# Kernel tuning notes

Hardware: AMD Instinct MI355X
Metric: run time of the kernel (lower is better)

The kernel has to match this reference:

```python
import jax, jax.numpy as jnp
import numpy as np
import math

B, L, X, E, Y = 2, 1024, 4, 128, 4  # batch, win_size/seq, search heads, head dim, retrieval heads


def setup_inputs() -> dict:
    key = jax.random.key(0)
    ks = jax.random.split(key, 12)
    f = jnp.float32
    x = jax.random.normal(ks[0], (B, L, X, E), f)
    query = jax.random.normal(ks[1], (B, L, X, E), f)
    k = jax.random.normal(ks[2], (B, L, X, E), f)
    value = jax.random.normal(ks[3], (B, L, Y, E), f)
    sigma = jax.random.normal(ks[4], (B, L, X), f)
    q_plus = jax.random.normal(ks[5], (B, L, X, E), f)
    # custom triangular mask over (search, retrieval) dims, broadcastable to scores [B,L,M,X,Y]
    attn_mask = jnp.triu(jnp.ones((X, Y), dtype=bool), k=1)
    # Linear(E,E) params (key_plus projection and V projection)
    s = 1.0 / math.sqrt(E)
    Wk = jax.random.normal(ks[6], (E, E), f) * s
    bk = jax.random.normal(ks[7], (E,), f) * s
    Wv = jax.random.normal(ks[8], (E, E), f) * s
    bv = jax.random.normal(ks[9], (E,), f) * s
    return {"x": x, "query": query, "key": k, "value": value, "sigma": sigma,
            "attn_mask": attn_mask, "retrieval": Y, "search": X, "q_plus": q_plus,
            "Wk": Wk, "bk": bk, "Wv": Wv, "bv": bv}


def reference(x, query, key, value, sigma, attn_mask, retrieval, search, q_plus, Wk, bk, Wv, bv):
    Bq, Lq, Hq, Eq = query.shape
    scale = 1.0 / math.sqrt(Eq)
    # stage 1: search attention over keys, per search-head x
    Search = jax.nn.softmax(jnp.einsum('blxe,bsxe->bxls', query, key) * scale, axis=-1)  # [B,X,L,S]
    Retrieval = jnp.einsum('bxls,bsye->blexy', Search, value)  # [B,L,E,X,Y]
    # key_plus = Linear(E,E) over the E axis of Retrieval
    key_plus = jnp.einsum('blexy,fe->blfxy', Retrieval, Wk) + bk[None, None, :, None, None]  # [B,L,E,X,Y]
    # stage 2: scores between q_plus and retrieved keys
    scores = jnp.einsum('blxe,bmexy->blmxy', q_plus, key_plus)  # [B,L,M,X,Y]
    scores = jnp.where(attn_mask[None, None, None, :, :], -jnp.inf, scores)
    series = jax.nn.softmax(scores * scale, axis=-1)  # softmax over Y (retrieval)
    # sigma transform -> Gaussian prior over |i-j| distances
    sig = jnp.transpose(sigma, (0, 2, 1))               # [B,Hs,L]
    sig = jax.nn.sigmoid(sig * 5.0) + 1e-5
    sig = jnp.power(3.0, sig) - 1.0
    sig = sig[..., None]                                # [B,Hs,L,1]
    idx = jnp.arange(Lq, dtype=jnp.float32)
    dist = jnp.abs(idx[:, None] - idx[None, :])         # [L,L]
    prior = 1.0 / (np.float32(math.sqrt(2.0 * math.pi)) * sig) * jnp.exp(-dist ** 2 / 2.0 / sig ** 2)  # [B,Hs,L,L]
    # dropout p=0.0 -> identity
    catt = jnp.einsum('blsxy,bsexy->blexy', series, Retrieval)  # [B,L,E,X,Y]
    V = jnp.sum(catt, axis=-1)                           # chunk over Y then sum -> [B,L,E,X]
    V_list = V.reshape(Bq, Lq, search, -1)               # row-major reinterpret == torch .view
    V = jnp.einsum('blse,fe->blsf', V_list, Wv) + bv     # [B,L,search,E]
    series_out = jnp.mean(jnp.transpose(series, (0, 3, 1, 2, 4)), axis=-1)  # chunk/sum/retrieval == mean over Y -> [B,X,L,M]
    return V, series_out, prior, sig
```

## Files before the change

### kernel.cpp

```cpp
#include <hip/hip_runtime.h>
#include <math.h>

#define B 2
#define L 1024
#define X 4
#define E 128
#define Y 4
#define SCALE 0.08838834764831845f

typedef unsigned short u16;
typedef __attribute__((ext_vector_type(8))) short bf16frag;
typedef __attribute__((ext_vector_type(4))) float floatx4;

static __device__ __forceinline__ u16 bfr(float f) {
  union { float f; unsigned u; } c; c.f = f;
  unsigned r = (c.u + 0x7fffu + ((c.u >> 16) & 1u)) >> 16;
  return (u16)r;
}

__global__ __launch_bounds__(256) void k_prep(const float* __restrict__ q,
                                              const float* __restrict__ key,
                                              const float* __restrict__ value,
                                              const float* __restrict__ sigma,
                                              const float* __restrict__ Wv,
                                              float4* __restrict__ sout4,
                                              u16* __restrict__ qkb,
                                              float* __restrict__ colsum,
                                              u16* __restrict__ vt,
                                              float4* __restrict__ wv4t,
                                              float* __restrict__ prior,
                                              float* __restrict__ sigout) {
  __shared__ float shp[2];
  const int bid = blockIdx.x;
  const int t = threadIdx.x;
  if (bid < 8192) {
    sout4[bid * 256 + t] = make_float4(0.25f, 0.25f, 0.25f, 0.25f);
  } else if (bid < 8208) {
    const int idx = (bid - 8192) * 256 + t;
    const int e4 = idx >> 7, f = idx & 127;
    wv4t[idx] = *(const float4*)(Wv + f * E + e4 * 4);
  } else if (bid < 9232) {
    if (bid == 8208) colsum[t] = 0.f;
    const int f = (bid - 8208) * 256 + t;
    const int row = f >> 4, c8 = (f & 15) * 8;
    const int sel = row >> 13, row2 = row & 8191;
    const int b = row2 >> 12, l = (row2 >> 2) & 1023, x = row2 & 3;
    const float* src = (sel ? key : q) + (size_t)row2 * E + c8;
    float4 v0 = *(const float4*)src;
    float4 v1 = *(const float4*)(src + 4);
    u16 us[8] = {bfr(v0.x), bfr(v0.y), bfr(v0.z), bfr(v0.w),
                 bfr(v1.x), bfr(v1.y), bfr(v1.z), bfr(v1.w)};
    u16* dst = qkb + (size_t)(sel * 8192 + (b * 4 + x) * 1024 + l) * E + c8;
    *(uint4*)dst = *(uint4*)us;
  } else if (bid < 9360) {
    const int blk = bid - 9232;
    const int by = blk >> 4, sc2 = blk & 15;
    const int b = by >> 2, y = by & 3;
    const int e = t & 127, sh = t >> 7;
    const int s0 = sc2 * 64 + sh * 32;
    u16 us[32];
#pragma unroll 8
    for (int ss = 0; ss < 32; ++ss)
      us[ss] = bfr(value[((size_t)((b * L + s0 + ss) * Y + y)) * E + e]);
    u16* dst = vt + ((size_t)(by * E + e)) * L + s0;
#pragma unroll
    for (int i = 0; i < 4; ++i) *(uint4*)(dst + i * 8) = *(uint4*)&us[i * 8];
  } else {
    const int row = bid - 9360;
    const int bx = row >> 10;
    const int i = row & 1023;
    const int b = bx >> 2, x = bx & 3;
    if (t == 0) {
      const double sv = (double)sigma[((size_t)(b * L + i)) * X + x];
      const double sg = 1.0 / (1.0 + exp(-5.0 * sv)) + 1e-5;
      const double s3 = exp(sg * 1.0986122886681098) - 1.0;
      shp[0] = (float)(1.0 / (2.5066282746310002 * s3));
      shp[1] = (float)(0.5 / (s3 * s3));
      sigout[row] = (float)s3;
    }
    __syncthreads();
    const float coef = shp[0], inv2s2 = shp[1];
    const float di = (float)i;
    const int j0 = t * 4;
    float4 o; float d;
    d = di - (float)(j0 + 0); o.x = coef * __expf(-d * d * inv2s2);
    d = di - (float)(j0 + 1); o.y = coef * __expf(-d * d * inv2s2);
    d = di - (float)(j0 + 2); o.z = coef * __expf(-d * d * inv2s2);
    d = di - (float)(j0 + 3); o.w = coef * __expf(-d * d * inv2s2);
    *(float4*)(prior + (size_t)row * 1024 + j0) = o;
  }
}

__global__ __launch_bounds__(512) void k1_mfma(const u16* __restrict__ qb,
                                               const u16* __restrict__ kb,
                                               u16* __restrict__ sbh,
                                               float* __restrict__ isum) {
  __shared__ __align__(16) u16 Qt[16][136];
  __shared__ __align__(16) u16 Kt[128][136];
  __shared__ float red[8][16];
  const int t = threadIdx.x;
  const int blk = blockIdx.x;
  const int lt = blk & 63, bx = blk >> 6;
  const int l0 = lt * 16;
  const int lane = t & 63, w = t >> 6;
  const int col = lane & 15, quad = lane >> 4;
  if (t < 256) {
    const int r = t >> 4, c8 = (t & 15) * 8;
    *(uint4*)&Qt[r][c8] = *(const uint4*)(qb + (size_t)(bx * L + l0 + r) * E + c8);
  }
  __syncthreads();
  bf16frag af[4];
#pragma unroll
  for (int k = 0; k < 4; ++k)
    af[k] = *(const bf16frag*)&Qt[col][k * 32 + quad * 8];

  float rs[4] = {0.f, 0.f, 0.f, 0.f};
  for (int sc = 0; sc < 8; ++sc) {
    __syncthreads();
    {
      const int r = t >> 2, c = (t & 3) * 32;
      const u16* src = kb + (size_t)(bx * L + sc * 128 + r) * E + c;
#pragma unroll
      for (int i = 0; i < 4; ++i)
        *(uint4*)&Kt[r][c + i * 8] = *(const uint4*)(src + i * 8);
    }
    __syncthreads();
    floatx4 acc = (floatx4){0.f, 0.f, 0.f, 0.f};
#pragma unroll
    for (int k = 0; k < 4; ++k) {
      bf16frag bk = *(const bf16frag*)&Kt[w * 16 + col][k * 32 + quad * 8];
      acc = __builtin_amdgcn_mfma_f32_16x16x32_bf16(af[k], bk, acc, 0, 0, 0);
    }
    const size_t so = (size_t)sc * 128 + w * 16 + col;
#pragma unroll
    for (int r = 0; r < 4; ++r) {
      float p = __expf(acc[r] * SCALE);
      rs[r] += p;
      sbh[(size_t)(bx * L + l0 + quad * 4 + r) * L + so] = bfr(p);
    }
  }
#pragma unroll
  for (int m = 1; m <= 8; m <<= 1)
#pragma unroll
    for (int r = 0; r < 4; ++r) rs[r] += __shfl_xor(rs[r], m, 64);
  __syncthreads();
  if (col == 0)
#pragma unroll
    for (int r = 0; r < 4; ++r) red[w][quad * 4 + r] = rs[r];
  __syncthreads();
  if (w == 0 && col == 0)
#pragma unroll
    for (int r = 0; r < 4; ++r) {
      float s = 0.f;
#pragma unroll
      for (int j = 0; j < 8; ++j) s += red[j][quad * 4 + r];
      isum[bx * L + l0 + quad * 4 + r] = 1.0f / s;
    }
}

__global__ __launch_bounds__(256) void k34_retr_kp(const u16* __restrict__ sbh,
                                                   const u16* __restrict__ vt,
                                                   const float* __restrict__ isum,
                                                   const float* __restrict__ Wk,
                                                   const float* __restrict__ bk,
                                                   u16* __restrict__ kp_bf,
                                                   u16* __restrict__ rt_bf,
                                                   float* __restrict__ colsum) {
  __shared__ __align__(16) unsigned char smem[23040];
  u16 (*Pt)[72] = (u16(*)[72])smem;
  u16 (*Vt)[72] = (u16(*)[72])(smem + 4608);
  float (*Rt)[132] = (float(*)[132])smem;
  const int t = threadIdx.x;
  const int blk = (blockIdx.x & 7) * 80 + (blockIdx.x >> 3);
  const int lt = blk & 31;
  const int cp = blk >> 5;
  const int b = cp / 10, p = cp % 10;
  const int x = (p >= 6) ? 3 : (p >= 3) ? 2 : (p >= 1) ? 1 : 0;
  const int y = p - ((x * (x + 1)) >> 1);
  const int by = b * 4 + y;
  const int srow = (b * 4 + x) * L;
  const int l0 = lt * 32;
  const int lane = t & 63, w = t >> 6;
  const int col = lane & 15, quad = lane >> 4;
  const int lw = w >> 1, eg = w & 1;
  floatx4 vf[4];
#pragma unroll
  for (int i = 0; i < 4; ++i) vf[i] = (floatx4){0.f, 0.f, 0.f, 0.f};
  for (int sc2 = 0; sc2 < 16; ++sc2) {
    const int s0 = sc2 * 64;
    __syncthreads();
    {
      const int r = t >> 3, c8 = (t & 7) * 8;
      *(uint4*)&Pt[r][c8] = *(const uint4*)(sbh + (size_t)(srow + l0 + r) * L + s0 + c8);
    }
    {
      const int e = t >> 1, off = (t & 1) * 32;
      const u16* src = vt + ((size_t)(by * E + e)) * L + s0 + off;
#pragma unroll
      for (int i = 0; i < 4; ++i)
        *(uint4*)&Vt[e][off + i * 8] = *(const uint4*)(src + i * 8);
    }
    __syncthreads();
#pragma unroll
    for (int ks = 0; ks < 2; ++ks) {
      bf16frag pf = *(const bf16frag*)&Pt[lw * 16 + col][ks * 32 + quad * 8];
#pragma unroll
      for (int i = 0; i < 4; ++i) {
        bf16frag rf = *(const bf16frag*)&Vt[(eg * 4 + i) * 16 + col][ks * 32 + quad * 8];
        vf[i] = __builtin_amdgcn_mfma_f32_16x16x32_bf16(pf, rf, vf[i], 0, 0, 0);
      }
    }
  }
  float is[4];
#pragma unroll
  for (int r = 0; r < 4; ++r) is[r] = isum[srow + l0 + lw * 16 + quad * 4 + r];
  __syncthreads();
#pragma unroll
  for (int i = 0; i < 4; ++i)
#pragma unroll
    for (int r = 0; r < 4; ++r)
      Rt[lw * 16 + quad * 4 + r][(eg * 4 + i) * 16 + col] = vf[i][r] * is[r];
  __syncthreads();
  if (p == 0) {
    if (t < 128) {
      float ssum = 0.f;
#pragma unroll
      for (int r = 0; r < 32; ++r) ssum += Rt[r][t];
      atomicAdd(&colsum[b * 128 + t], ssum);
    }
    return;
  }
  const int cslot = b * 9 + (p - 1);
  bf16frag aR[4];
#pragma unroll
  for (int k = 0; k < 4; ++k) {
    u16 us[8];
#pragma unroll
    for (int j = 0; j < 8; ++j) us[j] = bfr(Rt[lw * 16 + col][k * 32 + quad * 8 + j]);
    aR[k] = *(bf16frag*)us;
  }
#pragma unroll
  for (int ft = 0; ft < 4; ++ft) {
    const int f0 = (eg * 4 + ft) * 16;
    floatx4 c = (floatx4){0.f, 0.f, 0.f, 0.f};
#pragma unroll
    for (int k = 0; k < 4; ++k) {
      const float* wr = Wk + (size_t)(f0 + col) * E + k * 32 + quad * 8;
      float4 w0 = *(const float4*)wr;
      float4 w1 = *(const float4*)(wr + 4);
      u16 us[8] = {bfr(w0.x), bfr(w0.y), bfr(w0.z), bfr(w0.w),
                   bfr(w1.x), bfr(w1.y), bfr(w1.z), bfr(w1.w)};
      bf16frag bf = *(bf16frag*)us;
      c = __builtin_amdgcn_mfma_f32_16x16x32_bf16(aR[k], bf, c, 0, 0, 0);
    }
    const float bias = bk[f0 + col];
#pragma unroll
    for (int r = 0; r < 4; ++r)
      kp_bf[((size_t)(cslot * L + l0 + lw * 16 + quad * 4 + r)) * E + f0 + col] =
          bfr(c[r] + bias);
  }
  {
    const int e = t >> 1, half = t & 1;
    u16 us[16];
#pragma unroll
    for (int j = 0; j < 16; ++j) us[j] = bfr(Rt[half * 16 + j][e]);
    u16* dst = rt_bf + ((size_t)(cslot * E + e)) * L + l0 + half * 16;
    *(uint4*)dst = *(uint4*)&us[0];
    *(uint4*)(dst + 8) = *(uint4*)&us[8];
  }
}

template<int NY>
static __device__ __forceinline__ void k5_body(const float* __restrict__ qp,
                                               const u16* __restrict__ kp_bf,
                                               const u16* __restrict__ rt_bf,
                                               float* __restrict__ vws,
                                               u16 (*__restrict__ uni)[128][40],
                                               u16 (*__restrict__ pT)[32][40],
                                               const int t, const int b,
                                               const int lt, const int part,
                                               const int slotbase) {
  constexpr int x = NY - 1;
  u16 (*kpT)[32][136] = (u16 (*)[32][136])uni;
  const int mc0 = part * 4;
  const int l0 = lt * 32;
  const int lane = t & 63, w = t >> 6;
  const int col = lane & 15, quad = lane >> 4;
  const int lw = w >> 1, mt = w & 1, eg = w & 1;
  const int smr = t >> 3, se0 = (t & 7) * 16;
  const int sre = t >> 1, srh = (t & 1) * 16;

  bf16frag af[4];
  {
    const float* qpr = qp + ((size_t)((b * L + l0 + lw * 16 + col) * X + x)) * E;
#pragma unroll
    for (int k = 0; k < 4; ++k) {
      float4 v0 = *(const float4*)(qpr + k * 32 + quad * 8);
      float4 v1 = *(const float4*)(qpr + k * 32 + quad * 8 + 4);
      u16 us[8] = {bfr(v0.x), bfr(v0.y), bfr(v0.z), bfr(v0.w),
                   bfr(v1.x), bfr(v1.y), bfr(v1.z), bfr(v1.w)};
      af[k] = *(bf16frag*)us;
    }
  }
  floatx4 vf[4];
#pragma unroll
  for (int i = 0; i < 4; ++i) vf[i] = (floatx4){0.f, 0.f, 0.f, 0.f};

  for (int mc = mc0; mc < mc0 + 4; ++mc) {
    const int m0 = mc * 32;
    __syncthreads();
#pragma unroll
    for (int y = 0; y < NY; ++y) {
      const u16* src = kp_bf + ((size_t)(slotbase + y) * L + m0 + smr) * E + se0;
      uint4 a0 = *(const uint4*)src;
      uint4 a1 = *(const uint4*)(src + 8);
      *(uint4*)&kpT[y][smr][se0] = a0;
      *(uint4*)&kpT[y][smr][se0 + 8] = a1;
    }
    __syncthreads();
    floatx4 sf[NY];
#pragma unroll
    for (int y = 0; y < NY; ++y) sf[y] = (floatx4){0.f, 0.f, 0.f, 0.f};
#pragma unroll
    for (int y = 0; y < NY; ++y)
#pragma unroll
      for (int k = 0; k < 4; ++k) {
        bf16frag bkf = *(const bf16frag*)&kpT[y][mt * 16 + col][k * 32 + quad * 8];
        sf[y] = __builtin_amdgcn_mfma_f32_16x16x32_bf16(af[k], bkf, sf[y], 0, 0, 0);
      }
    u16 pu[NY][4];
#pragma unroll
    for (int r = 0; r < 4; ++r) {
      float zz[NY]; float mx = -3.4e38f;
#pragma unroll
      for (int y = 0; y < NY; ++y) { zz[y] = sf[y][r] * SCALE; mx = fmaxf(mx, zz[y]); }
      float sum = 0.f;
#pragma unroll
      for (int y = 0; y < NY; ++y) { zz[y] = __expf(zz[y] - mx); sum += zz[y]; }
      float inv = 1.0f / sum;
#pragma unroll
      for (int y = 0; y < NY; ++y) pu[y][r] = bfr(zz[y] * inv);
    }
    __syncthreads();
#pragma unroll
    for (int y = 0; y < NY; ++y) {
#pragma unroll
      for (int r = 0; r < 4; ++r)
        pT[y][lw * 16 + quad * 4 + r][mt * 16 + col] = pu[y][r];
      const u16* src = rt_bf + ((size_t)(slotbase + y) * E + sre) * L + m0 + srh;
      uint4 a0 = *(const uint4*)src;
      uint4 a1 = *(const uint4*)(src + 8);
      *(uint4*)&uni[y][sre][srh] = a0;
      *(uint4*)&uni[y][sre][srh + 8] = a1;
    }
    __syncthreads();
#pragma unroll
    for (int y = 0; y < NY; ++y) {
      bf16frag pf = *(const bf16frag*)&pT[y][lw * 16 + col][quad * 8];
#pragma unroll
      for (int i = 0; i < 4; ++i) {
        bf16frag rf = *(const bf16frag*)&uni[y][(eg * 4 + i) * 16 + col][quad * 8];
        vf[i] = __builtin_amdgcn_mfma_f32_16x16x32_bf16(pf, rf, vf[i], 0, 0, 0);
      }
    }
  }
  float* dst = vws + (size_t)(b * 24 + (x - 1) * 8 + part) * (L * E) + (size_t)l0 * E;
#pragma unroll
  for (int i = 0; i < 4; ++i)
#pragma unroll
    for (int r = 0; r < 4; ++r)
      dst[((size_t)(lw * 16 + quad * 4 + r)) * E + (eg * 4 + i) * 16 + col] = vf[i][r];
}

__global__ __launch_bounds__(256) void k5_stage2(const float* __restrict__ qp,
                                                 const u16* __restrict__ kp_bf,
                                                 const u16* __restrict__ rt_bf,
                                                 float* __restrict__ vws) {
  __shared__ __align__(16) u16 uni[4][128][40];
  __shared__ __align__(16) u16 pT[4][32][40];
  const int t = threadIdx.x;
  const int vb = (blockIdx.x & 7) * 192 + (blockIdx.x >> 3);
  const int g = vb >> 8;
  const int r = vb & 255;
  const int b = g / 3, xm1 = g % 3;
  const int part = r >> 5, lt = r & 31;
  const int slotbase = b * 9 + ((xm1 == 0) ? 0 : (xm1 == 1) ? 2 : 5);
  if (xm1 == 0)      k5_body<2>(qp, kp_bf, rt_bf, vws, uni, pT, t, b, lt, part, slotbase);
  else if (xm1 == 1) k5_body<3>(qp, kp_bf, rt_bf, vws, uni, pT, t, b, lt, part, slotbase);
  else               k5_body<4>(qp, kp_bf, rt_bf, vws, uni, pT, t, b, lt, part, slotbase);
}

__global__ __launch_bounds__(256) void k6_vout(const float* __restrict__ vws,
                                               const float4* __restrict__ wv4t,
                                               const float* __restrict__ bv,
                                               const float* __restrict__ colsum,
                                               float* __restrict__ vout) {
  __shared__ __align__(16) float rowf[8][512];
  const int t = threadIdx.x;
  const int blk = blockIdx.x;
  const int bl0 = blk * 8;
  const int b = bl0 >> 10;
  const int lbase = bl0 & 1023;
  {
    const int o = t * 2;
    const int xh = o >> 7, e = o & 127;
    if (xh == 0) {
      const float sx = colsum[b * 128 + e];
      const float sy = colsum[b * 128 + e + 1];
#pragma unroll
      for (int l8 = 0; l8 < 8; ++l8) {
        rowf[l8][e * 4] = sx;
        rowf[l8][(e + 1) * 4] = sy;
      }
    } else {
      const size_t pbase = (size_t)(b * 24 + (xh - 1) * 8) * 131072;
#pragma unroll
      for (int l8 = 0; l8 < 8; ++l8) {
        const size_t base = pbase + (size_t)(lbase + l8) * 128 + e;
        float sx = 0.f, sy = 0.f;
#pragma unroll
        for (int p = 0; p < 8; ++p) {
          float2 v = *(const float2*)(vws + base + (size_t)p * 131072);
          sx += v.x; sy += v.y;
        }
        rowf[l8][e * 4 + xh] = sx;
        rowf[l8][(e + 1) * 4 + xh] = sy;
      }
    }
  }
  __syncthreads();
#pragma unroll
  for (int rep = 0; rep < 2; ++rep) {
    const int o = t + rep * 256;
    const int s = o >> 7, f = o & 127;
    float acc[8] = {0.f, 0.f, 0.f, 0.f, 0.f, 0.f, 0.f, 0.f};
    const float4* wp = wv4t + f;
#pragma unroll 4
    for (int e4 = 0; e4 < 32; ++e4) {
      const float4 wv = wp[e4 * 128];
#pragma unroll
      for (int l8 = 0; l8 < 8; ++l8) {
        const float4 rv = *(const float4*)&rowf[l8][(s * 32 + e4) * 4];
        acc[l8] += wv.x * rv.x + wv.y * rv.y + wv.z * rv.z + wv.w * rv.w;
      }
    }
    const float bb = bv[f];
#pragma unroll
    for (int l8 = 0; l8 < 8; ++l8)
      vout[(size_t)(bl0 + l8) * 512 + s * 128 + f] = acc[l8] + bb;
  }
}

extern "C" void kernel_launch(void* const* d_in, const int* in_sizes, int n_in,
                              void* d_out, int out_size, void* d_ws, size_t ws_size,
                              hipStream_t stream) {
  const float* q     = (const float*)d_in[1];
  const float* key   = (const float*)d_in[2];
  const float* value = (const float*)d_in[3];
  const float* sigma = (const float*)d_in[4];
  const float* qp    = (const float*)d_in[8];
  const float* Wk    = (const float*)d_in[9];
  const float* bk    = (const float*)d_in[10];
  const float* Wv    = (const float*)d_in[11];
  const float* bv    = (const float*)d_in[12];

  float* out    = (float*)d_out;
  float* Vout   = out;
  float* sout   = out + 1048576;
  float* prior  = out + 9437184;
  float* sigout = out + 17825792;

  float* ws     = (float*)d_ws;
  u16*   sbh    = (u16*)ws;
  u16*   qb     = (u16*)(ws + 4194304);
  u16*   kb     = qb + 1048576;
  u16*   vt     = (u16*)(ws + 5242880);
  float* isum   = ws + 5767168;
  float* wv4t   = ws + 6291456;
  u16*   kp_bf  = (u16*)(ws + 8388608);
  u16*   rt_bf  = (u16*)(ws + 9568256);
  float* colsum = ws + 10747904;
  float* vws    = ws;

  hipLaunchKernelGGL(k_prep,      dim3(17552), dim3(256), 0, stream, q, key, value, sigma,
                     Wv, (float4*)sout, (u16*)qb, colsum, vt, (float4*)wv4t, prior, sigout);
  hipLaunchKernelGGL(k1_mfma,     dim3(512),  dim3(512), 0, stream, qb, kb, sbh, isum);
  hipLaunchKernelGGL(k34_retr_kp, dim3(640),  dim3(256), 0, stream, sbh, vt, isum, Wk, bk, kp_bf, rt_bf, colsum);
  hipLaunchKernelGGL(k5_stage2,   dim3(1536), dim3(256), 0, stream, qp, kp_bf, rt_bf, vws);
  hipLaunchKernelGGL(k6_vout,     dim3(256),  dim3(256), 0, stream, vws, (const float4*)wv4t, bv, colsum, Vout);
}
```

Before: 210.2 us.

## Rebalance stage-2 work split across heads and pre-pack Wk as bf16 MFMA fragments

The stage-2 kernel previously gave every search head 8 partial chunks of 4 m-tiles, even though heads with fewer active retrieval slots cost less per tile. The new split gives 4, 6 and 8 partials to the three heads, with uneven chunk lengths, so blocks do more similar amounts of work, and the launch drops from 1536 to 1152 blocks. The final reduction kernel now reads a variable number of partials per head. Separately, Wk is converted to bf16 once in the prep kernel in MFMA fragment order, instead of being loaded and converted inside every k34 block. The cost is longer per-block runtimes in stage 2 and a few extra prep blocks.

```diff
diff --git a/kernel.cpp b/kernel.cpp
--- a/kernel.cpp
+++ b/kernel.cpp
@@ -23,11 +23,13 @@
                                               const float* __restrict__ value,
                                               const float* __restrict__ sigma,
                                               const float* __restrict__ Wv,
+                                              const float* __restrict__ Wk,
                                               float4* __restrict__ sout4,
                                               u16* __restrict__ qkb,
                                               float* __restrict__ colsum,
                                               u16* __restrict__ vt,
                                               float4* __restrict__ wv4t,
+                                              u16* __restrict__ wkf,
                                               float* __restrict__ prior,
                                               float* __restrict__ sigout) {
   __shared__ float shp[2];
@@ -65,7 +67,7 @@
     u16* dst = vt + ((size_t)(by * E + e)) * L + s0;
 #pragma unroll
     for (int i = 0; i < 4; ++i) *(uint4*)(dst + i * 8) = *(uint4*)&us[i * 8];
-  } else {
+  } else if (bid < 17552) {
     const int row = bid - 9360;
     const int bx = row >> 10;
     const int i = row & 1023;
@@ -88,6 +90,17 @@
     d = di - (float)(j0 + 2); o.z = coef * __expf(-d * d * inv2s2);
     d = di - (float)(j0 + 3); o.w = coef * __expf(-d * d * inv2s2);
     *(float4*)(prior + (size_t)row * 1024 + j0) = o;
+  } else {
+    const int idx = (bid - 17552) * 256 + t;
+    const int slot = idx >> 6, lane2 = idx & 63;
+    const int col = lane2 & 15, quad = lane2 >> 4;
+    const int eg = slot >> 4, ft = (slot >> 2) & 3, k = slot & 3;
+    const float* src = Wk + (size_t)((eg * 4 + ft) * 16 + col) * E + k * 32 + quad * 8;
+    float4 w0 = *(const float4*)src;
+    float4 w1 = *(const float4*)(src + 4);
+    u16 us[8] = {bfr(w0.x), bfr(w0.y), bfr(w0.z), bfr(w0.w),
+                 bfr(w1.x), bfr(w1.y), bfr(w1.z), bfr(w1.w)};
+    *(uint4*)(wkf + (size_t)idx * 8) = *(uint4*)us;
   }
 }
 
@@ -161,7 +174,7 @@
 __global__ __launch_bounds__(256) void k34_retr_kp(const u16* __restrict__ sbh,
                                                    const u16* __restrict__ vt,
                                                    const float* __restrict__ isum,
-                                                   const float* __restrict__ Wk,
+                                                   const u16* __restrict__ wkf,
                                                    const float* __restrict__ bk,
                                                    u16* __restrict__ kp_bf,
                                                    u16* __restrict__ rt_bf,
@@ -245,12 +258,7 @@
     floatx4 c = (floatx4){0.f, 0.f, 0.f, 0.f};
 #pragma unroll
     for (int k = 0; k < 4; ++k) {
-      const float* wr = Wk + (size_t)(f0 + col) * E + k * 32 + quad * 8;
-      float4 w0 = *(const float4*)wr;
-      float4 w1 = *(const float4*)(wr + 4);
-      u16 us[8] = {bfr(w0.x), bfr(w0.y), bfr(w0.z), bfr(w0.w),
-                   bfr(w1.x), bfr(w1.y), bfr(w1.z), bfr(w1.w)};
-      bf16frag bf = *(bf16frag*)us;
+      bf16frag bf = *(const bf16frag*)&wkf[(size_t)((((eg * 4 + ft) * 4 + k) * 64) + lane) * 8];
       c = __builtin_amdgcn_mfma_f32_16x16x32_bf16(aR[k], bf, c, 0, 0, 0);
     }
     const float bias = bk[f0 + col];
@@ -278,11 +286,11 @@
                                                u16 (*__restrict__ uni)[128][40],
                                                u16 (*__restrict__ pT)[32][40],
                                                const int t, const int b,
-                                               const int lt, const int part,
+                                               const int lt, const int mc0,
+                                               const int mcCnt, const int vslot,
                                                const int slotbase) {
   constexpr int x = NY - 1;
   u16 (*kpT)[32][136] = (u16 (*)[32][136])uni;
-  const int mc0 = part * 4;
   const int l0 = lt * 32;
   const int lane = t & 63, w = t >> 6;
   const int col = lane & 15, quad = lane >> 4;
@@ -306,7 +314,7 @@
 #pragma unroll
   for (int i = 0; i < 4; ++i) vf[i] = (floatx4){0.f, 0.f, 0.f, 0.f};
 
-  for (int mc = mc0; mc < mc0 + 4; ++mc) {
+  for (int mc = mc0; mc < mc0 + mcCnt; ++mc) {
     const int m0 = mc * 32;
     __syncthreads();
 #pragma unroll
@@ -364,7 +372,7 @@
       }
     }
   }
-  float* dst = vws + (size_t)(b * 24 + (x - 1) * 8 + part) * (L * E) + (size_t)l0 * E;
+  float* dst = vws + (size_t)vslot * (L * E) + (size_t)l0 * E;
 #pragma unroll
   for (int i = 0; i < 4; ++i)
 #pragma unroll
@@ -379,15 +387,22 @@
   __shared__ __align__(16) u16 uni[4][128][40];
   __shared__ __align__(16) u16 pT[4][32][40];
   const int t = threadIdx.x;
-  const int vb = (blockIdx.x & 7) * 192 + (blockIdx.x >> 3);
-  const int g = vb >> 8;
-  const int r = vb & 255;
-  const int b = g / 3, xm1 = g % 3;
-  const int part = r >> 5, lt = r & 31;
-  const int slotbase = b * 9 + ((xm1 == 0) ? 0 : (xm1 == 1) ? 2 : 5);
-  if (xm1 == 0)      k5_body<2>(qp, kp_bf, rt_bf, vws, uni, pT, t, b, lt, part, slotbase);
-  else if (xm1 == 1) k5_body<3>(qp, kp_bf, rt_bf, vws, uni, pT, t, b, lt, part, slotbase);
-  else               k5_body<4>(qp, kp_bf, rt_bf, vws, uni, pT, t, b, lt, part, slotbase);
+  const int vb = (blockIdx.x & 7) * 144 + (blockIdx.x >> 3);
+  const int b = vb / 576;
+  const int rem = vb % 576;
+  const int g18 = rem >> 5, lt = rem & 31;
+  int x, part, mc0, cnt, off;
+  if (g18 < 4)       { x = 1; part = g18;      mc0 = part * 8; cnt = 8; off = 0; }
+  else if (g18 < 10) { x = 2; part = g18 - 4;
+                       if (part < 4) { mc0 = 5 * part; cnt = 5; }
+                       else          { mc0 = 20 + 6 * (part - 4); cnt = 6; }
+                       off = 4; }
+  else               { x = 3; part = g18 - 10; mc0 = part * 4; cnt = 4; off = 10; }
+  const int slotbase = b * 9 + ((x == 1) ? 0 : (x == 2) ? 2 : 5);
+  const int vslot = b * 18 + off + part;
+  if (x == 1)      k5_body<2>(qp, kp_bf, rt_bf, vws, uni, pT, t, b, lt, mc0, cnt, vslot, slotbase);
+  else if (x == 2) k5_body<3>(qp, kp_bf, rt_bf, vws, uni, pT, t, b, lt, mc0, cnt, vslot, slotbase);
+  else             k5_body<4>(qp, kp_bf, rt_bf, vws, uni, pT, t, b, lt, mc0, cnt, vslot, slotbase);
 }
 
 __global__ __launch_bounds__(256) void k6_vout(const float* __restrict__ vws,
@@ -413,13 +428,16 @@
         rowf[l8][(e + 1) * 4] = sy;
       }
     } else {
-      const size_t pbase = (size_t)(b * 24 + (xh - 1) * 8) * 131072;
+      int np, off;
+      if (xh == 1)      { np = 4; off = 0; }
+      else if (xh == 2) { np = 6; off = 4; }
+      else              { np = 8; off = 10; }
+      const size_t pbase = (size_t)(b * 18 + off) * 131072;
 #pragma unroll
       for (int l8 = 0; l8 < 8; ++l8) {
         const size_t base = pbase + (size_t)(lbase + l8) * 128 + e;
         float sx = 0.f, sy = 0.f;
-#pragma unroll
-        for (int p = 0; p < 8; ++p) {
+        for (int p = 0; p < np; ++p) {
           float2 v = *(const float2*)(vws + base + (size_t)p * 131072);
           sx += v.x; sy += v.y;
         }
@@ -477,15 +495,16 @@
   u16*   vt     = (u16*)(ws + 5242880);
   float* isum   = ws + 5767168;
   float* wv4t   = ws + 6291456;
+  u16*   wkf    = (u16*)(ws + 6307840);
   u16*   kp_bf  = (u16*)(ws + 8388608);
   u16*   rt_bf  = (u16*)(ws + 9568256);
   float* colsum = ws + 10747904;
   float* vws    = ws;
 
-  hipLaunchKernelGGL(k_prep,      dim3(17552), dim3(256), 0, stream, q, key, value, sigma,
-                     Wv, (float4*)sout, (u16*)qb, colsum, vt, (float4*)wv4t, prior, sigout);
+  hipLaunchKernelGGL(k_prep,      dim3(17560), dim3(256), 0, stream, q, key, value, sigma,
+                     Wv, Wk, (float4*)sout, (u16*)qb, colsum, vt, (float4*)wv4t, wkf, prior, sigout);
   hipLaunchKernelGGL(k1_mfma,     dim3(512),  dim3(512), 0, stream, qb, kb, sbh, isum);
-  hipLaunchKernelGGL(k34_retr_kp, dim3(640),  dim3(256), 0, stream, sbh, vt, isum, Wk, bk, kp_bf, rt_bf, colsum);
-  hipLaunchKernelGGL(k5_stage2,   dim3(1536), dim3(256), 0, stream, qp, kp_bf, rt_bf, vws);
+  hipLaunchKernelGGL(k34_retr_kp, dim3(640),  dim3(256), 0, stream, sbh, vt, isum, wkf, bk, kp_bf, rt_bf, colsum);
+  hipLaunchKernelGGL(k5_stage2,   dim3(1152), dim3(256), 0, stream, qp, kp_bf, rt_bf, vws);
   hipLaunchKernelGGL(k6_vout,     dim3(256),  dim3(256), 0, stream, vws, (const float4*)wv4t, bv, colsum, Vout);
 }
```

Result: slower. 221.0 us (+5.1%).
